# Kernel tuning notes

Hardware: AMD Instinct MI355X
Metric: run time of the kernel (lower is better)

The kernel has to match this reference:

```python
import jax, jax.numpy as jnp
import numpy as np

D_MODEL = 1024
NUM_HEADS = 16
DEPTH = D_MODEL // NUM_HEADS


def setup_inputs() -> dict:
    key = jax.random.key(0)
    ks = jax.random.split(key, 11)
    B, S = 4, 2048
    scale = 1.0 / np.sqrt(D_MODEL)
    inp = {
        "query": jax.random.normal(ks[0], (B, S, D_MODEL), jnp.float32),
        "key": jax.random.normal(ks[1], (B, S, D_MODEL), jnp.float32),
        "value": jax.random.normal(ks[2], (B, S, D_MODEL), jnp.float32),
        # Linear params (torch nn.Linear: y = x @ W.T + b); store W as [out, in]
        "wq_w": jax.random.normal(ks[3], (D_MODEL, D_MODEL), jnp.float32) * scale,
        "wq_b": jnp.zeros((D_MODEL,), jnp.float32),
        "wk_w": jax.random.normal(ks[4], (D_MODEL, D_MODEL), jnp.float32) * scale,
        "wk_b": jnp.zeros((D_MODEL,), jnp.float32),
        "wv_w": jax.random.normal(ks[5], (D_MODEL, D_MODEL), jnp.float32) * scale,
        "wv_b": jnp.zeros((D_MODEL,), jnp.float32),
        "dense_w": jax.random.normal(ks[6], (D_MODEL, D_MODEL), jnp.float32) * scale,
        "dense_b": jnp.zeros((D_MODEL,), jnp.float32),
    }
    return inp


def _split_heads(x, B):
    # [B, S, D] -> [B, H, S, depth]
    return x.reshape(B, -1, NUM_HEADS, DEPTH).transpose(0, 2, 1, 3)


def reference(query, key, value, wq_w, wq_b, wk_w, wk_b, wv_w, wv_b, dense_w, dense_b):
    B = query.shape[0]
    q = _split_heads(query @ wq_w.T + wq_b, B)   # [B,H,Sq,depth]
    k = _split_heads(key @ wk_w.T + wk_b, B)     # [B,H,Sk,depth]
    v = _split_heads(value @ wv_w.T + wv_b, B)   # [B,H,Sk,depth]
    scores = jnp.einsum("bhqd,bhkd->bhqk", q, k) / jnp.sqrt(jnp.float32(DEPTH)).astype(q.dtype)
    attn = jax.nn.softmax(scores, axis=-1)
    out = jnp.einsum("bhqk,bhkd->bhqd", attn, v)  # [B,H,Sq,depth]
    out = out.transpose(0, 2, 1, 3).reshape(B, -1, D_MODEL)
    return out @ dense_w.T + dense_b
```

## Files before the change

kernel.cpp:

```cpp
#include <hip/hip_runtime.h>
#include <hip/hip_bf16.h>
#include <stdint.h>


#define SEQ    2048
#define DEPTH  64
#define HEADS  16
#define NMODEL 1024
#define MROWS  8192

typedef __bf16 bf16x8 __attribute__((ext_vector_type(8)));
typedef __bf16 bf16x4 __attribute__((ext_vector_type(4)));
typedef float  f32x4  __attribute__((ext_vector_type(4)));

__device__ __forceinline__ unsigned short f32_bf16(float f) {
    union { float f; unsigned int u; } c; c.f = f;
    unsigned int u = c.u + 0x7FFFu + ((c.u >> 16) & 1u);
    return (unsigned short)(u >> 16);
}

__device__ __forceinline__ void gload16(const unsigned short* g, unsigned short* l) {
    __builtin_amdgcn_global_load_lds(
        (const __attribute__((address_space(1))) unsigned int*)g,
        (__attribute__((address_space(3))) unsigned int*)l, 16, 0, 0);
}

__global__ __launch_bounds__(256) void cvt3_kernel(
    const float* __restrict__ a, const float* __restrict__ b, const float* __restrict__ c,
    unsigned short* __restrict__ oa, unsigned short* __restrict__ ob,
    unsigned short* __restrict__ oc, int n4)
{
    const float* in; unsigned short* out;
    if (blockIdx.y == 0) { in = a; out = oa; }
    else if (blockIdx.y == 1) { in = b; out = ob; }
    else { in = c; out = oc; }
    int i = blockIdx.x * 256 + threadIdx.x;
    if (i < n4) {
        float4 f = ((const float4*)in)[i];
        ushort4 o;
        o.x = f32_bf16(f.x); o.y = f32_bf16(f.y);
        o.z = f32_bf16(f.z); o.w = f32_bf16(f.w);
        ((ushort4*)out)[i] = o;
    }
}

__global__ __launch_bounds__(256) void cvt4_kernel(
    const float* __restrict__ a, const float* __restrict__ b,
    const float* __restrict__ c, const float* __restrict__ d,
    unsigned short* __restrict__ oa, unsigned short* __restrict__ ob,
    unsigned short* __restrict__ oc, unsigned short* __restrict__ od, int n4)
{
    const float* in; unsigned short* out;
    if (blockIdx.y == 0) { in = a; out = oa; }
    else if (blockIdx.y == 1) { in = b; out = ob; }
    else if (blockIdx.y == 2) { in = c; out = oc; }
    else { in = d; out = od; }
    int i = blockIdx.x * 256 + threadIdx.x;
    if (i < n4) {
        float4 f = ((const float4*)in)[i];
        ushort4 o;
        o.x = f32_bf16(f.x); o.y = f32_bf16(f.y);
        o.z = f32_bf16(f.z); o.w = f32_bf16(f.w);
        ((ushort4*)out)[i] = o;
    }
}

__device__ __forceinline__ void gemm128_core(
    const unsigned short* __restrict__ A, const unsigned short* __restrict__ W,
    const float* __restrict__ bias, void* __restrict__ outp,
    int mode, float scale, int m0, int n0,
    unsigned short* Alds, unsigned short* Blds)
{
    const int tid  = threadIdx.x;
    const int wave = tid >> 6, lane = tid & 63;
    const int l15  = lane & 15, quad = lane >> 4;
    const int wm   = wave & 1,  wn   = wave >> 1;
    const int swz  = l15 & 7;
    const int K    = 1024;

    f32x4 acc[4][4] = {};

    const int lrow = lane >> 3;
    const int fcol = ((lane & 7) ^ lrow) << 3;
    const unsigned short* Ab[4];
    const unsigned short* Bb[4];
    #pragma unroll
    for (int c = 0; c < 4; ++c) {
        const int seg = 4 * wave + c;
        Ab[c] = A + (size_t)(m0 + seg * 8 + lrow) * K + fcol;
        Bb[c] = W + (size_t)(n0 + seg * 8 + lrow) * K + fcol;
    }

    for (int k0 = 0; k0 < K; k0 += 64) {
        #pragma unroll
        for (int c = 0; c < 4; ++c) {
            gload16(Ab[c] + k0, &Alds[(4 * wave + c) * 512]);
            gload16(Bb[c] + k0, &Blds[(4 * wave + c) * 512]);
        }
        __syncthreads();

        #pragma unroll
        for (int kc = 0; kc < 2; ++kc) {
            bf16x8 a[4], b[4];
            const int pg = (((kc * 4 + quad) ^ swz) << 3);
            #pragma unroll
            for (int i = 0; i < 4; ++i)
                a[i] = *(const bf16x8*)&Alds[(wm * 64 + i * 16 + l15) * 64 + pg];
            #pragma unroll
            for (int j = 0; j < 4; ++j)
                b[j] = *(const bf16x8*)&Blds[(wn * 64 + j * 16 + l15) * 64 + pg];
            #pragma unroll
            for (int i = 0; i < 4; ++i)
                #pragma unroll
                for (int j = 0; j < 4; ++j)
                    acc[i][j] = __builtin_amdgcn_mfma_f32_16x16x32_bf16(a[i], b[j], acc[i][j], 0, 0, 0);
        }
        __syncthreads();
    }

    #pragma unroll
    for (int i = 0; i < 4; ++i) {
        #pragma unroll
        for (int j = 0; j < 4; ++j) {
            const int col = n0 + wn * 64 + j * 16 + l15;
            const int row_b = m0 + wm * 64 + i * 16 + quad * 4;
            if (mode == 2) {
                #pragma unroll
                for (int r = 0; r < 4; ++r) {
                    const int row = row_b + r;
                    ((unsigned short*)outp)[(size_t)row * MROWS + col] =
                        f32_bf16(acc[i][j][r] + bias[row]);
                }
            } else if (mode == 0) {
                const float bv = bias[col];
                #pragma unroll
                for (int r = 0; r < 4; ++r)
                    ((float*)outp)[(size_t)(row_b + r) * NMODEL + col] = acc[i][j][r] + bv;
            } else {
                const float bv = bias[col];
                const int h_ = col >> 6, d_ = col & 63;
                #pragma unroll
                for (int r = 0; r < 4; ++r) {
                    const int row = row_b + r;
                    const int b_ = row >> 11, s_ = row & 2047;
                    ((unsigned short*)outp)[(((size_t)(b_ * HEADS + h_) * SEQ + s_) << 6) + d_] =
                        f32_bf16((acc[i][j][r] + bv) * scale);
                }
            }
        }
    }
}

__global__ __launch_bounds__(256, 3) void gemm_qkv(
    const unsigned short* __restrict__ qb,  const unsigned short* __restrict__ wqb,
    const float* __restrict__ bq, unsigned short* __restrict__ Qp,
    const unsigned short* __restrict__ kb,  const unsigned short* __restrict__ wkb,
    const float* __restrict__ bk, unsigned short* __restrict__ Kpj,
    const unsigned short* __restrict__ wvb, const unsigned short* __restrict__ vb,
    const float* __restrict__ bv, unsigned short* __restrict__ Vtg,
    float qscale)
{
    __shared__ unsigned short Alds[128 * 64];
    __shared__ unsigned short Blds[128 * 64];
    const int bid = blockIdx.x, z = blockIdx.y;
    if (z == 0) {
        gemm128_core(qb, wqb, bq, Qp, 1, qscale, (bid >> 3) * 128, (bid & 7) * 128, Alds, Blds);
    } else if (z == 1) {
        gemm128_core(kb, wkb, bk, Kpj, 1, 1.0f, (bid >> 3) * 128, (bid & 7) * 128, Alds, Blds);
    } else {
        gemm128_core(wvb, vb, bv, Vtg, 2, 1.0f, (bid & 7) * 128, (bid >> 3) * 128, Alds, Blds);
    }
}

__global__ __launch_bounds__(256, 3) void gemm_dense(
    const unsigned short* __restrict__ A, const unsigned short* __restrict__ W,
    const float* __restrict__ bias, float* __restrict__ out)
{
    __shared__ unsigned short Alds[128 * 64];
    __shared__ unsigned short Blds[128 * 64];
    const int bid = blockIdx.x;
    gemm128_core(A, W, bias, out, 0, 1.0f, (bid >> 3) * 128, (bid & 7) * 128, Alds, Blds);
}

__global__ __launch_bounds__(256, 4) void attn_fwd(
    const unsigned short* __restrict__ Qp,
    const unsigned short* __restrict__ Kp,
    const unsigned short* __restrict__ Vtg,
    unsigned short* __restrict__ Op)
{
    __shared__ unsigned short Klds[2 * 64 * 64];
    __shared__ unsigned short Vlds[2 * 64 * 64];
    const int tid  = threadIdx.x;
    const int wave = tid >> 6, lane = tid & 63;
    const int l15  = lane & 15, quad = lane >> 4;
    const int swz  = l15 & 7;
    const int bh   = blockIdx.y;
    const int b_   = bh >> 4, h_ = bh & 15;
    const int q0   = blockIdx.x * 128;

    const unsigned short* Qb = Qp + (size_t)bh * SEQ * DEPTH;
    const unsigned short* Kb = Kp + (size_t)bh * SEQ * DEPTH;
    const unsigned short* Vb = Vtg + (size_t)h_ * DEPTH * MROWS + (size_t)b_ * SEQ;

    const int srow = (wave << 3) + (lane >> 3);
    const int scg  = (lane & 7) ^ ((lane >> 3) & 7);

    const unsigned short* Kg0 = Kb + (size_t)srow * DEPTH + scg * 8;
    const unsigned short* Kg1 = Kb + (size_t)(srow + 32) * DEPTH + scg * 8;
    const unsigned short* Vg0 = Vb + (size_t)srow * MROWS + scg * 8;
    const unsigned short* Vg1 = Vb + (size_t)(srow + 32) * MROWS + scg * 8;

    bf16x8 qf[2][2];
    #pragma unroll
    for (int i = 0; i < 2; ++i)
        #pragma unroll
        for (int kc = 0; kc < 2; ++kc)
            qf[i][kc] = *(const bf16x8*)(Qb + (size_t)(q0 + wave * 32 + i * 16 + l15) * DEPTH
                                         + kc * 32 + quad * 8);

    union { bf16x8 v; unsigned short s[8]; } uo;
    #pragma unroll
    for (int j = 0; j < 8; ++j) uo.s[j] = 0x3F80;
    const bf16x8 ones = uo.v;

    f32x4 Ot[2][4] = {};
    f32x4 lacc[2]  = {};

    auto STAGE = [&](int buf, int kt) {
        unsigned short* KW = &Klds[buf * 4096 + wave * 512];
        unsigned short* VW = &Vlds[buf * 4096 + wave * 512];
        gload16(Kg0 + (size_t)kt * 4096, KW);
        gload16(Kg1 + (size_t)kt * 4096, KW + 2048);
        gload16(Vg0 + kt * 64, VW);
        gload16(Vg1 + kt * 64, VW + 2048);
    };

    STAGE(0, 0);
    asm volatile("s_waitcnt vmcnt(0)" ::: "memory");
    __builtin_amdgcn_s_barrier();

    for (int kt = 0; kt < SEQ / 64; ++kt) {
        const int cur = kt & 1;
        if (kt + 1 < SEQ / 64) STAGE(cur ^ 1, kt + 1);

        const unsigned short* Kc = &Klds[cur * 4096];
        const unsigned short* Vc = &Vlds[cur * 4096];

        f32x4 St[2][4] = {};
        #pragma unroll
        for (int jj = 0; jj < 4; ++jj) {
            bf16x8 k0 = *(const bf16x8*)&Kc[(jj * 16 + l15) * 64 + ((quad ^ swz) << 3)];
            bf16x8 k1 = *(const bf16x8*)&Kc[(jj * 16 + l15) * 64 + (((4 + quad) ^ swz) << 3)];
            St[0][jj] = __builtin_amdgcn_mfma_f32_16x16x32_bf16(k0, qf[0][0], St[0][jj], 0, 0, 0);
            St[0][jj] = __builtin_amdgcn_mfma_f32_16x16x32_bf16(k1, qf[0][1], St[0][jj], 0, 0, 0);
            St[1][jj] = __builtin_amdgcn_mfma_f32_16x16x32_bf16(k0, qf[1][0], St[1][jj], 0, 0, 0);
            St[1][jj] = __builtin_amdgcn_mfma_f32_16x16x32_bf16(k1, qf[1][1], St[1][jj], 0, 0, 0);
        }

        #pragma unroll
        for (int i = 0; i < 2; ++i)
            #pragma unroll
            for (int jj = 0; jj < 4; ++jj)
                #pragma unroll
                for (int r = 0; r < 4; ++r)
                    St[i][jj][r] = __builtin_amdgcn_exp2f(St[i][jj][r]);

        bf16x8 pf[2][2];
        #pragma unroll
        for (int i = 0; i < 2; ++i)
            #pragma unroll
            for (int kc = 0; kc < 2; ++kc) {
                union { bf16x8 v; __hip_bfloat162 h[4]; } up;
                up.h[0] = __float22bfloat162_rn(make_float2(St[i][2 * kc][0],     St[i][2 * kc][1]));
                up.h[1] = __float22bfloat162_rn(make_float2(St[i][2 * kc][2],     St[i][2 * kc][3]));
                up.h[2] = __float22bfloat162_rn(make_float2(St[i][2 * kc + 1][0], St[i][2 * kc + 1][1]));
                up.h[3] = __float22bfloat162_rn(make_float2(St[i][2 * kc + 1][2], St[i][2 * kc + 1][3]));
                pf[i][kc] = up.v;
            }

        lacc[0] = __builtin_amdgcn_mfma_f32_16x16x32_bf16(ones, pf[0][0], lacc[0], 0, 0, 0);
        lacc[0] = __builtin_amdgcn_mfma_f32_16x16x32_bf16(ones, pf[0][1], lacc[0], 0, 0, 0);
        lacc[1] = __builtin_amdgcn_mfma_f32_16x16x32_bf16(ones, pf[1][0], lacc[1], 0, 0, 0);
        lacc[1] = __builtin_amdgcn_mfma_f32_16x16x32_bf16(ones, pf[1][1], lacc[1], 0, 0, 0);

        #pragma unroll
        for (int kc = 0; kc < 2; ++kc) {
            const int glo = ((kc * 4 + (quad >> 1)) ^ swz);
            const int ghi = ((kc * 4 + 2 + (quad >> 1)) ^ swz);
            const int sub = (quad & 1) * 4;
            #pragma unroll
            for (int dd = 0; dd < 4; ++dd) {
                const int row = (dd * 16 + l15) * 64;
                union { bf16x8 v; bf16x4 h[2]; } uv;
                uv.h[0] = *(const bf16x4*)&Vc[row + glo * 8 + sub];
                uv.h[1] = *(const bf16x4*)&Vc[row + ghi * 8 + sub];
                Ot[0][dd] = __builtin_amdgcn_mfma_f32_16x16x32_bf16(uv.v, pf[0][kc], Ot[0][dd], 0, 0, 0);
                Ot[1][dd] = __builtin_amdgcn_mfma_f32_16x16x32_bf16(uv.v, pf[1][kc], Ot[1][dd], 0, 0, 0);
            }
        }

        asm volatile("s_waitcnt vmcnt(0)" ::: "memory");
        __builtin_amdgcn_s_barrier();
    }

    #pragma unroll
    for (int i = 0; i < 2; ++i) {
        const float inv = 1.0f / lacc[i][0];
        const int row = b_ * SEQ + q0 + wave * 32 + i * 16 + l15;
        #pragma unroll
        for (int dd = 0; dd < 4; ++dd) {
            ushort4 ov;
            ov.x = f32_bf16(Ot[i][dd][0] * inv);
            ov.y = f32_bf16(Ot[i][dd][1] * inv);
            ov.z = f32_bf16(Ot[i][dd][2] * inv);
            ov.w = f32_bf16(Ot[i][dd][3] * inv);
            const int col = h_ * 64 + dd * 16 + quad * 4;
            *(ushort4*)&Op[(size_t)row * NMODEL + col] = ov;
        }
    }
}

extern "C" void kernel_launch(void* const* d_in, const int* in_sizes, int n_in,
                              void* d_out, int out_size, void* d_ws, size_t ws_size,
                              hipStream_t stream) {
    const float* q  = (const float*)d_in[0];
    const float* k  = (const float*)d_in[1];
    const float* v  = (const float*)d_in[2];
    const float* wq = (const float*)d_in[3];
    const float* bq = (const float*)d_in[4];
    const float* wk = (const float*)d_in[5];
    const float* bk = (const float*)d_in[6];
    const float* wv = (const float*)d_in[7];
    const float* bv = (const float*)d_in[8];
    const float* wd = (const float*)d_in[9];
    const float* bd = (const float*)d_in[10];

    char* ws = (char*)d_ws;
    size_t off = 0;
    auto alloc = [&](size_t bytes) { char* p = ws + off; off += bytes; return p; };
    const size_t ACT = (size_t)MROWS * NMODEL * 2;
    const size_t WGT = (size_t)NMODEL * NMODEL * 2;

    unsigned short* qb   = (unsigned short*)alloc(ACT);
    unsigned short* kb   = (unsigned short*)alloc(ACT);
    unsigned short* vb   = (unsigned short*)alloc(ACT);
    unsigned short* wqb  = (unsigned short*)alloc(WGT);
    unsigned short* wkb  = (unsigned short*)alloc(WGT);
    unsigned short* wvb  = (unsigned short*)alloc(WGT);
    unsigned short* wdb  = (unsigned short*)alloc(WGT);
    unsigned short* Qp   = (unsigned short*)alloc(ACT);
    unsigned short* Kpj  = (unsigned short*)alloc(ACT);
    unsigned short* Vtg  = (unsigned short*)alloc(ACT);
    unsigned short* attn = (unsigned short*)alloc(ACT);

    const int nAct4 = MROWS * NMODEL / 4;
    const int nWgt4 = NMODEL * NMODEL / 4;
    cvt3_kernel<<<dim3(nAct4 / 256, 3), 256, 0, stream>>>(q, k, v, qb, kb, vb, nAct4);
    cvt4_kernel<<<dim3(nWgt4 / 256, 4), 256, 0, stream>>>(wq, wk, wv, wd,
                                                          wqb, wkb, wvb, wdb, nWgt4);

    const float SC = 0.18033688011112042f;
    gemm_qkv<<<dim3(512, 3), 256, 0, stream>>>(qb, wqb, bq, Qp,
                                               kb, wkb, bk, Kpj,
                                               wvb, vb, bv, Vtg, SC);

    attn_fwd<<<dim3(SEQ / 128, 64), 256, 0, stream>>>(Qp, Kpj, Vtg, attn);

    gemm_dense<<<512, 256, 0, stream>>>(attn, wdb, bd, (float*)d_out);
}
```

Baseline: 330.0 us.

## Double per-wave query rows in attention, permute V columns for 16-byte loads

The attention kernel now gives each wave 64 query rows instead of 32, so each block covers 256 queries and each K/V tile in LDS is reused across twice as many rows. The V projection epilogue permutes columns within 32-element groups so the attention kernel can read V fragments with one 16-byte LDS load instead of two 8-byte loads. The score, exp and PV steps are split into two halves of 32 keys to limit register pressure, with s_setprio hints around the MFMA sections. Occupancy drops from 4 to 2 blocks per CU and the grid is halved, which risks less latency hiding.

```diff
diff --git a/kernel.cpp b/kernel.cpp
--- a/kernel.cpp
+++ b/kernel.cpp
@@ -10,7 +10,6 @@
 #define MROWS  8192
 
 typedef __bf16 bf16x8 __attribute__((ext_vector_type(8)));
-typedef __bf16 bf16x4 __attribute__((ext_vector_type(4)));
 typedef float  f32x4  __attribute__((ext_vector_type(4)));
 
 __device__ __forceinline__ unsigned short f32_bf16(float f) {
@@ -125,10 +124,14 @@
             const int col = n0 + wn * 64 + j * 16 + l15;
             const int row_b = m0 + wm * 64 + i * 16 + quad * 4;
             if (mode == 2) {
+                const int colp = (col & ~31)
+                               | (col & 3)
+                               | (((col >> 4) & 1) << 2)
+                               | (((col >> 2) & 3) << 3);
                 #pragma unroll
                 for (int r = 0; r < 4; ++r) {
                     const int row = row_b + r;
-                    ((unsigned short*)outp)[(size_t)row * MROWS + col] =
+                    ((unsigned short*)outp)[(size_t)row * MROWS + colp] =
                         f32_bf16(acc[i][j][r] + bias[row]);
                 }
             } else if (mode == 0) {
@@ -182,7 +185,7 @@
     gemm128_core(A, W, bias, out, 0, 1.0f, (bid >> 3) * 128, (bid & 7) * 128, Alds, Blds);
 }
 
-__global__ __launch_bounds__(256, 4) void attn_fwd(
+__global__ __launch_bounds__(256, 2) void attn_fwd(
     const unsigned short* __restrict__ Qp,
     const unsigned short* __restrict__ Kp,
     const unsigned short* __restrict__ Vtg,
@@ -196,7 +199,7 @@
     const int swz  = l15 & 7;
     const int bh   = blockIdx.y;
     const int b_   = bh >> 4, h_ = bh & 15;
-    const int q0   = blockIdx.x * 128;
+    const int q0   = blockIdx.x * 256;
 
     const unsigned short* Qb = Qp + (size_t)bh * SEQ * DEPTH;
     const unsigned short* Kb = Kp + (size_t)bh * SEQ * DEPTH;
@@ -210,12 +213,12 @@
     const unsigned short* Vg0 = Vb + (size_t)srow * MROWS + scg * 8;
     const unsigned short* Vg1 = Vb + (size_t)(srow + 32) * MROWS + scg * 8;
 
-    bf16x8 qf[2][2];
-    #pragma unroll
-    for (int i = 0; i < 2; ++i)
+    bf16x8 qf[4][2];
+    #pragma unroll
+    for (int i = 0; i < 4; ++i)
         #pragma unroll
         for (int kc = 0; kc < 2; ++kc)
-            qf[i][kc] = *(const bf16x8*)(Qb + (size_t)(q0 + wave * 32 + i * 16 + l15) * DEPTH
+            qf[i][kc] = *(const bf16x8*)(Qb + (size_t)(q0 + wave * 64 + i * 16 + l15) * DEPTH
                                          + kc * 32 + quad * 8);
 
     union { bf16x8 v; unsigned short s[8]; } uo;
@@ -223,8 +226,8 @@
     for (int j = 0; j < 8; ++j) uo.s[j] = 0x3F80;
     const bf16x8 ones = uo.v;
 
-    f32x4 Ot[2][4] = {};
-    f32x4 lacc[2]  = {};
+    f32x4 Ot[4][4] = {};
+    f32x4 lacc[4]  = {};
 
     auto STAGE = [&](int buf, int kt) {
         unsigned short* KW = &Klds[buf * 4096 + wave * 512];
@@ -244,59 +247,61 @@
         if (kt + 1 < SEQ / 64) STAGE(cur ^ 1, kt + 1);
 
         const unsigned short* Kc = &Klds[cur * 4096];
-        const unsigned short* Vc = &Vlds[cur * 4096];
-
-        f32x4 St[2][4] = {};
-        #pragma unroll
-        for (int jj = 0; jj < 4; ++jj) {
-            bf16x8 k0 = *(const bf16x8*)&Kc[(jj * 16 + l15) * 64 + ((quad ^ swz) << 3)];
-            bf16x8 k1 = *(const bf16x8*)&Kc[(jj * 16 + l15) * 64 + (((4 + quad) ^ swz) << 3)];
-            St[0][jj] = __builtin_amdgcn_mfma_f32_16x16x32_bf16(k0, qf[0][0], St[0][jj], 0, 0, 0);
-            St[0][jj] = __builtin_amdgcn_mfma_f32_16x16x32_bf16(k1, qf[0][1], St[0][jj], 0, 0, 0);
-            St[1][jj] = __builtin_amdgcn_mfma_f32_16x16x32_bf16(k0, qf[1][0], St[1][jj], 0, 0, 0);
-            St[1][jj] = __builtin_amdgcn_mfma_f32_16x16x32_bf16(k1, qf[1][1], St[1][jj], 0, 0, 0);
-        }
-
-        #pragma unroll
-        for (int i = 0; i < 2; ++i)
-            #pragma unroll
-            for (int jj = 0; jj < 4; ++jj)
-                #pragma unroll
-                for (int r = 0; r < 4; ++r)
-                    St[i][jj][r] = __builtin_amdgcn_exp2f(St[i][jj][r]);
-
-        bf16x8 pf[2][2];
-        #pragma unroll
-        for (int i = 0; i < 2; ++i)
-            #pragma unroll
-            for (int kc = 0; kc < 2; ++kc) {
+
+        #pragma unroll
+        for (int half = 0; half < 2; ++half) {
+            __builtin_amdgcn_s_setprio(1);
+            const int r0 = (2 * half) * 16 + l15;
+            const int r1 = (2 * half + 1) * 16 + l15;
+            bf16x8 ka0 = *(const bf16x8*)&Kc[r0 * 64 + ((quad ^ swz) << 3)];
+            bf16x8 ka1 = *(const bf16x8*)&Kc[r0 * 64 + (((4 + quad) ^ swz) << 3)];
+            bf16x8 kb0 = *(const bf16x8*)&Kc[r1 * 64 + ((quad ^ swz) << 3)];
+            bf16x8 kb1 = *(const bf16x8*)&Kc[r1 * 64 + (((4 + quad) ^ swz) << 3)];
+            f32x4 S0[4], S1[4];
+            #pragma unroll
+            for (int i = 0; i < 4; ++i) {
+                S0[i] = f32x4{};
+                S0[i] = __builtin_amdgcn_mfma_f32_16x16x32_bf16(ka0, qf[i][0], S0[i], 0, 0, 0);
+                S0[i] = __builtin_amdgcn_mfma_f32_16x16x32_bf16(ka1, qf[i][1], S0[i], 0, 0, 0);
+                S1[i] = f32x4{};
+                S1[i] = __builtin_amdgcn_mfma_f32_16x16x32_bf16(kb0, qf[i][0], S1[i], 0, 0, 0);
+                S1[i] = __builtin_amdgcn_mfma_f32_16x16x32_bf16(kb1, qf[i][1], S1[i], 0, 0, 0);
+            }
+            __builtin_amdgcn_s_setprio(0);
+
+            bf16x8 pfh[4];
+            #pragma unroll
+            for (int i = 0; i < 4; ++i) {
+                float e0 = __builtin_amdgcn_exp2f(S0[i][0]);
+                float e1 = __builtin_amdgcn_exp2f(S0[i][1]);
+                float e2 = __builtin_amdgcn_exp2f(S0[i][2]);
+                float e3 = __builtin_amdgcn_exp2f(S0[i][3]);
+                float e4 = __builtin_amdgcn_exp2f(S1[i][0]);
+                float e5 = __builtin_amdgcn_exp2f(S1[i][1]);
+                float e6 = __builtin_amdgcn_exp2f(S1[i][2]);
+                float e7 = __builtin_amdgcn_exp2f(S1[i][3]);
                 union { bf16x8 v; __hip_bfloat162 h[4]; } up;
-                up.h[0] = __float22bfloat162_rn(make_float2(St[i][2 * kc][0],     St[i][2 * kc][1]));
-                up.h[1] = __float22bfloat162_rn(make_float2(St[i][2 * kc][2],     St[i][2 * kc][3]));
-                up.h[2] = __float22bfloat162_rn(make_float2(St[i][2 * kc + 1][0], St[i][2 * kc + 1][1]));
-                up.h[3] = __float22bfloat162_rn(make_float2(St[i][2 * kc + 1][2], St[i][2 * kc + 1][3]));
-                pf[i][kc] = up.v;
+                up.h[0] = __float22bfloat162_rn(make_float2(e0, e1));
+                up.h[1] = __float22bfloat162_rn(make_float2(e2, e3));
+                up.h[2] = __float22bfloat162_rn(make_float2(e4, e5));
+                up.h[3] = __float22bfloat162_rn(make_float2(e6, e7));
+                pfh[i] = up.v;
             }
 
-        lacc[0] = __builtin_amdgcn_mfma_f32_16x16x32_bf16(ones, pf[0][0], lacc[0], 0, 0, 0);
-        lacc[0] = __builtin_amdgcn_mfma_f32_16x16x32_bf16(ones, pf[0][1], lacc[0], 0, 0, 0);
-        lacc[1] = __builtin_amdgcn_mfma_f32_16x16x32_bf16(ones, pf[1][0], lacc[1], 0, 0, 0);
-        lacc[1] = __builtin_amdgcn_mfma_f32_16x16x32_bf16(ones, pf[1][1], lacc[1], 0, 0, 0);
-
-        #pragma unroll
-        for (int kc = 0; kc < 2; ++kc) {
-            const int glo = ((kc * 4 + (quad >> 1)) ^ swz);
-            const int ghi = ((kc * 4 + 2 + (quad >> 1)) ^ swz);
-            const int sub = (quad & 1) * 4;
+            __builtin_amdgcn_s_setprio(1);
+            lacc[0] = __builtin_amdgcn_mfma_f32_16x16x32_bf16(ones, pfh[0], lacc[0], 0, 0, 0);
+            lacc[1] = __builtin_amdgcn_mfma_f32_16x16x32_bf16(ones, pfh[1], lacc[1], 0, 0, 0);
+            lacc[2] = __builtin_amdgcn_mfma_f32_16x16x32_bf16(ones, pfh[2], lacc[2], 0, 0, 0);
+            lacc[3] = __builtin_amdgcn_mfma_f32_16x16x32_bf16(ones, pfh[3], lacc[3], 0, 0, 0);
             #pragma unroll
             for (int dd = 0; dd < 4; ++dd) {
-                const int row = (dd * 16 + l15) * 64;
-                union { bf16x8 v; bf16x4 h[2]; } uv;
-                uv.h[0] = *(const bf16x4*)&Vc[row + glo * 8 + sub];
-                uv.h[1] = *(const bf16x4*)&Vc[row + ghi * 8 + sub];
-                Ot[0][dd] = __builtin_amdgcn_mfma_f32_16x16x32_bf16(uv.v, pf[0][kc], Ot[0][dd], 0, 0, 0);
-                Ot[1][dd] = __builtin_amdgcn_mfma_f32_16x16x32_bf16(uv.v, pf[1][kc], Ot[1][dd], 0, 0, 0);
+                bf16x8 vf = *(const bf16x8*)&Vlds[cur * 4096 +
+                            (dd * 16 + l15) * 64 + (((half * 4 + quad) ^ swz) << 3)];
+                #pragma unroll
+                for (int i = 0; i < 4; ++i)
+                    Ot[i][dd] = __builtin_amdgcn_mfma_f32_16x16x32_bf16(vf, pfh[i], Ot[i][dd], 0, 0, 0);
             }
+            __builtin_amdgcn_s_setprio(0);
         }
 
         asm volatile("s_waitcnt vmcnt(0)" ::: "memory");
@@ -304,9 +309,9 @@
     }
 
     #pragma unroll
-    for (int i = 0; i < 2; ++i) {
+    for (int i = 0; i < 4; ++i) {
         const float inv = 1.0f / lacc[i][0];
-        const int row = b_ * SEQ + q0 + wave * 32 + i * 16 + l15;
+        const int row = b_ * SEQ + q0 + wave * 64 + i * 16 + l15;
         #pragma unroll
         for (int dd = 0; dd < 4; ++dd) {
             ushort4 ov;
@@ -364,7 +369,7 @@
                                                kb, wkb, bk, Kpj,
                                                wvb, vb, bv, Vtg, SC);
 
-    attn_fwd<<<dim3(SEQ / 128, 64), 256, 0, stream>>>(Qp, Kpj, Vtg, attn);
+    attn_fwd<<<dim3(SEQ / 256, 64), 256, 0, stream>>>(Qp, Kpj, Vtg, attn);
 
     gemm_dense<<<512, 256, 0, stream>>>(attn, wdb, bd, (float*)d_out);
 }
```

Measured after the change: 321.3 us. -2.6%, faster.
